# Kernel optimization log

Hardware: AMD Instinct MI355X
Metric: run time of the kernel (lower is better)

Reference implementation:

```python
import jax, jax.numpy as jnp
import numpy as np

GROUP_SIZE = 128


def setup_inputs() -> dict:
    key = jax.random.key(0)
    k1, k2, k3 = jax.random.split(key, 3)
    B, S, IN, OUT = 4, 8192, 1024, 1024
    x = jax.random.normal(k1, (B, S, IN), dtype=jnp.float32)
    weight = jax.random.normal(k2, (OUT, IN), dtype=jnp.float32) * 0.02
    bias = jax.random.normal(k3, (OUT,), dtype=jnp.float32) * 0.01
    return {"x": x, "weight": weight, "bias": bias}


def reference(x, weight, bias):
    """Quantized int8 path: quantize() + _forward_int8 of OneBitLinear.

    - weights binarized to +/-1 int8 (sign, with 0 -> -1, matching
      sign().clamp(min=0) bit packing then 2*bit-1)
    - per-group weight scales = group absmax, stored fp16 (as in quantize())
    - activations dynamically quantized per-token to int8
    - int32-accumulated GEMM, rescaled by x_scale * mean group scale per row
    """
    out_f, in_f = weight.shape
    ng = in_f // GROUP_SIZE
    w_g = weight.reshape(out_f, ng, GROUP_SIZE)
    # per-group absmax scales, cast fp16 -> fp32 to mimic fp16 storage
    scales = jnp.maximum(jnp.max(jnp.abs(w_g), axis=-1), 1e-8)
    scales = scales.astype(jnp.float16).astype(jnp.float32)  # [O, ng]
    # +/-1 int8 weights (sign>0 -> +1, else -1; zero maps to -1 like the packer)
    w_int8 = jnp.where(weight > 0, 1, -1).astype(jnp.int8)  # [O, I]

    # dynamic per-token activation quantization
    x_f = x.reshape(-1, in_f)  # [BT, I]
    x_scale = jnp.maximum(jnp.max(jnp.abs(x_f), axis=1, keepdims=True), 1e-8) / 127.0
    x_int8 = jnp.clip(jnp.round(x_f / x_scale), -128, 127).astype(jnp.int8)

    # int8 GEMM with int32 accumulation
    out_i32 = jnp.matmul(
        x_int8.astype(jnp.int32), w_int8.T.astype(jnp.int32)
    )  # [BT, O]

    w_scale_per_row = jnp.mean(scales, axis=1)  # [O]
    out_f32 = out_i32.astype(jnp.float32) * x_scale * w_scale_per_row[None, :]
    out_f32 = out_f32 + bias[None, :]
    return out_f32.reshape(*x.shape[:-1], out_f)
```

## Files before the change

kernel.cpp:

```cpp
#include <hip/hip_runtime.h>
#include <hip/hip_fp16.h>

#define K_DIM 1024
#define N_DIM 1024

typedef int v4i __attribute__((ext_vector_type(4)));

__device__ __forceinline__ void async_load16(const void* g, void* l) {
    __builtin_amdgcn_global_load_lds(
        (const __attribute__((address_space(1))) unsigned int*)g,
        (__attribute__((address_space(3))) unsigned int*)l,
        16, 0, 0);
}

__global__ __launch_bounds__(256) void prep_quant(const float* __restrict__ w,
                                                  const float* __restrict__ x,
                                                  signed char* __restrict__ wq,
                                                  float* __restrict__ wscale,
                                                  signed char* __restrict__ xq,
                                                  float* __restrict__ xs) {
    const int lane = threadIdx.x & 63;
    if (blockIdx.x < 256) {
        const int row = blockIdx.x * 4 + (threadIdx.x >> 6);
        const float4* wr = (const float4*)(w + (size_t)row * K_DIM);
        float4 v[4];
#pragma unroll
        for (int j = 0; j < 4; ++j) v[j] = wr[lane * 4 + j];

        float g = 0.f;
#pragma unroll
        for (int j = 0; j < 4; ++j) {
            g = fmaxf(g, fabsf(v[j].x)); g = fmaxf(g, fabsf(v[j].y));
            g = fmaxf(g, fabsf(v[j].z)); g = fmaxf(g, fabsf(v[j].w));
        }
        g = fmaxf(g, __shfl_xor(g, 1, 64));
        g = fmaxf(g, __shfl_xor(g, 2, 64));
        g = fmaxf(g, __shfl_xor(g, 4, 64));
        const float s = __half2float(__float2half(fmaxf(g, 1e-8f)));
        float t = s;
        t += __shfl_xor(t, 8, 64);
        t += __shfl_xor(t, 16, 64);
        t += __shfl_xor(t, 32, 64);
        if (lane == 0) wscale[row] = t * 0.125f;

        int pk[4];
#pragma unroll
        for (int j = 0; j < 4; ++j) {
            const int b0 = (v[j].x > 0.f) ? 1 : -1;
            const int b1 = (v[j].y > 0.f) ? 1 : -1;
            const int b2 = (v[j].z > 0.f) ? 1 : -1;
            const int b3 = (v[j].w > 0.f) ? 1 : -1;
            pk[j] = (b0 & 255) | ((b1 & 255) << 8) | ((b2 & 255) << 16) | (b3 << 24);
        }
        *(int4*)(wq + (size_t)row * K_DIM + lane * 16) = make_int4(pk[0], pk[1], pk[2], pk[3]);
    } else {
        const int row = (blockIdx.x - 256) * 4 + (threadIdx.x >> 6);
        const float4* xr = (const float4*)(x + (size_t)row * K_DIM);
        float4 v[4];
#pragma unroll
        for (int j = 0; j < 4; ++j) v[j] = xr[lane * 4 + j];

        float am = 0.f;
#pragma unroll
        for (int j = 0; j < 4; ++j) {
            am = fmaxf(am, fabsf(v[j].x)); am = fmaxf(am, fabsf(v[j].y));
            am = fmaxf(am, fabsf(v[j].z)); am = fmaxf(am, fabsf(v[j].w));
        }
#pragma unroll
        for (int off = 32; off >= 1; off >>= 1) am = fmaxf(am, __shfl_xor(am, off, 64));
        const float scale = fmaxf(am, 1e-8f) / 127.f;
        const float inv   = 1.0f / scale;

        int pk[4];
#pragma unroll
        for (int j = 0; j < 4; ++j) {
            const int b0 = (int)fminf(fmaxf(rintf(v[j].x * inv), -128.f), 127.f);
            const int b1 = (int)fminf(fmaxf(rintf(v[j].y * inv), -128.f), 127.f);
            const int b2 = (int)fminf(fmaxf(rintf(v[j].z * inv), -128.f), 127.f);
            const int b3 = (int)fminf(fmaxf(rintf(v[j].w * inv), -128.f), 127.f);
            pk[j] = (b0 & 255) | ((b1 & 255) << 8) | ((b2 & 255) << 16) | (b3 << 24);
        }
        *(int4*)(xq + (size_t)row * K_DIM + lane * 16) = make_int4(pk[0], pk[1], pk[2], pk[3]);
        if (lane == 0) xs[row] = scale;
    }
}

__global__ __launch_bounds__(512, 2) void gemm_i8(const signed char* __restrict__ A,
                                                  const signed char* __restrict__ Bw,
                                                  const float* __restrict__ xs,
                                                  const float* __restrict__ wscale,
                                                  const float* __restrict__ bias,
                                                  float* __restrict__ out) {
    extern __shared__ __align__(16) signed char Bl[];

    const int tid  = threadIdx.x;
    const int lane = tid & 63;
    const int wave = tid >> 6;
    const int wm   = wave >> 1;
    const int wn   = wave & 1;

    const int bid = blockIdx.x;
    const int xcd = bid & 7;
    const int u   = bid >> 3;
    const int mT  = xcd * 16 + (u >> 3);
    const int nT  = u & 7;
    const size_t mBase = (size_t)mT * 256;
    const int    nBase = nT * 128;

    const int brow   = tid >> 6;
    const int bchunk = (tid & 63) ^ brow;
    const signed char* Bg = Bw + (size_t)(nBase + brow) * K_DIM + bchunk * 16;
#pragma unroll
    for (int c = 0; c < 16; ++c)
        async_load16(Bg + (size_t)(c * 8) * K_DIM, Bl + c * 8192 + tid * 16);

    const int r16 = lane & 15;
    const int g   = lane >> 4;

    const signed char* Arow[4];
#pragma unroll
    for (int mf = 0; mf < 4; ++mf)
        Arow[mf] = A + (mBase + wm * 64 + mf * 16 + r16) * (size_t)K_DIM + g * 16;

    const int s7 = r16 & 7;
    int Bbase[4];
#pragma unroll
    for (int nf = 0; nf < 4; ++nf)
        Bbase[nf] = (wn * 64 + nf * 16 + r16) * 1024;

    __syncthreads();

    v4i acc[4][4] = {};

#pragma unroll
    for (int t = 0; t < 16; ++t) {
        v4i af[4], bf[4];
#pragma unroll
        for (int mf = 0; mf < 4; ++mf)
            af[mf] = *(const v4i*)(Arow[mf] + t * 64);
#pragma unroll
        for (int nf = 0; nf < 4; ++nf)
            bf[nf] = *(const v4i*)(Bl + Bbase[nf] + (((t * 4 + g) ^ s7) * 16));
#pragma unroll
        for (int mf = 0; mf < 4; ++mf)
#pragma unroll
            for (int nf = 0; nf < 4; ++nf)
                acc[mf][nf] = __builtin_amdgcn_mfma_i32_16x16x64_i8(
                    af[mf], bf[nf], acc[mf][nf], 0, 0, 0);
    }

    const int rq = g * 4;
    float xsr[4][4];
#pragma unroll
    for (int mf = 0; mf < 4; ++mf)
#pragma unroll
        for (int i = 0; i < 4; ++i)
            xsr[mf][i] = xs[mBase + wm * 64 + mf * 16 + rq + i];

#pragma unroll
    for (int nf = 0; nf < 4; ++nf) {
        const int col   = nBase + wn * 64 + nf * 16 + r16;
        const float wsc = wscale[col];
        const float bb  = bias[col];
#pragma unroll
        for (int mf = 0; mf < 4; ++mf) {
#pragma unroll
            for (int i = 0; i < 4; ++i) {
                const size_t row = mBase + wm * 64 + mf * 16 + rq + i;
                out[row * N_DIM + col] = (float)acc[mf][nf][i] * xsr[mf][i] * wsc + bb;
            }
        }
    }
}

extern "C" void kernel_launch(void* const* d_in, const int* in_sizes, int n_in,
                              void* d_out, int out_size, void* d_ws, size_t ws_size,
                              hipStream_t stream) {
    const float* x    = (const float*)d_in[0];
    const float* w    = (const float*)d_in[1];
    const float* bias = (const float*)d_in[2];
    float* out = (float*)d_out;

    const int BT = in_sizes[0] / K_DIM;

    char* ws = (char*)d_ws;
    signed char* xq     = (signed char*)ws;
    float*       xs     = (float*)(ws + (size_t)BT * K_DIM);
    signed char* wq     = (signed char*)(ws + (size_t)BT * K_DIM + (size_t)BT * 4);
    float*       wscale = (float*)((char*)wq + (size_t)N_DIM * K_DIM);

    static bool s_attr_set = false;
    if (!s_attr_set) {
        hipFuncSetAttribute((const void*)gemm_i8,
                            hipFuncAttributeMaxDynamicSharedMemorySize, 131072);
        s_attr_set = true;
    }

    prep_quant<<<256 + BT / 4, 256, 0, stream>>>(w, x, wq, wscale, xq, xs);
    gemm_i8<<<(BT / 256) * (N_DIM / 128), 512, 131072, stream>>>(xq, wq, xs, wscale, bias, out);
}
```

Measured before the change: 304.9 us.

## Restructure int8 GEMM into 256x256 tiles with triple-buffered LDS pipeline

The GEMM tile grows from 256x128 to 256x256 per block with 8 waves in a 2x4 layout. A is now staged through LDS instead of read directly from global memory, and the full-K B preload is replaced by a 3-stage ring of 64-wide K slices filled by async global-to-LDS loads. Loads are interleaved with MFMA phases using explicit barriers, waitcnt and setprio. The goal is to overlap memory with compute and improve reuse. In exchange it adds many barriers per iteration and higher register pressure from 32 accumulators per thread.

```diff
diff --git a/kernel.cpp b/kernel.cpp
--- a/kernel.cpp
+++ b/kernel.cpp
@@ -12,6 +12,12 @@
         (__attribute__((address_space(3))) unsigned int*)l,
         16, 0, 0);
 }
+
+#define BAR() do { asm volatile("" ::: "memory"); \
+                   __builtin_amdgcn_s_barrier();  \
+                   asm volatile("" ::: "memory"); } while (0)
+#define LGKM0() do { asm volatile("s_waitcnt lgkmcnt(0)" ::: "memory"); \
+                     __builtin_amdgcn_sched_barrier(0); } while (0)
 
 __global__ __launch_bounds__(256) void prep_quant(const float* __restrict__ w,
                                                   const float* __restrict__ x,
@@ -91,71 +97,127 @@
                                                   const float* __restrict__ wscale,
                                                   const float* __restrict__ bias,
                                                   float* __restrict__ out) {
-    extern __shared__ __align__(16) signed char Bl[];
+    extern __shared__ __align__(16) signed char lds[];
 
     const int tid  = threadIdx.x;
     const int lane = tid & 63;
     const int wave = tid >> 6;
-    const int wm   = wave >> 1;
-    const int wn   = wave & 1;
+    const int wm   = wave >> 2;
+    const int wn   = wave & 3;
 
     const int bid = blockIdx.x;
     const int xcd = bid & 7;
     const int u   = bid >> 3;
-    const int mT  = xcd * 16 + (u >> 3);
-    const int nT  = u & 7;
+    const int mT  = xcd * 16 + (u >> 2);
+    const int nT  = u & 3;
     const size_t mBase = (size_t)mT * 256;
-    const int    nBase = nT * 128;
-
-    const int brow   = tid >> 6;
-    const int bchunk = (tid & 63) ^ brow;
-    const signed char* Bg = Bw + (size_t)(nBase + brow) * K_DIM + bchunk * 16;
-#pragma unroll
-    for (int c = 0; c < 16; ++c)
-        async_load16(Bg + (size_t)(c * 8) * K_DIM, Bl + c * 8192 + tid * 16);
-
-    const int r16 = lane & 15;
-    const int g   = lane >> 4;
-
-    const signed char* Arow[4];
-#pragma unroll
-    for (int mf = 0; mf < 4; ++mf)
-        Arow[mf] = A + (mBase + wm * 64 + mf * 16 + r16) * (size_t)K_DIM + g * 16;
-
-    const int s7 = r16 & 7;
-    int Bbase[4];
+    const int    nBase = nT * 256;
+
+    const int srow = tid >> 2;
+    const int lc16 = ((tid & 3) ^ ((srow >> 1) & 3)) * 16;
+    const int dst  = tid * 16;
+    const signed char* Ag0 = A  + (mBase + srow) * K_DIM + lc16;
+    const signed char* Ag1 = Ag0 + (size_t)128 * K_DIM;
+    const signed char* Bg0 = Bw + (size_t)(nBase + srow) * K_DIM + lc16;
+    const signed char* Bg1 = Bg0 + (size_t)128 * K_DIM;
+
+#define SA0(b, kt) async_load16(Ag0 + (kt) * 64, lds + (b) * 32768 + dst)
+#define SA1(b, kt) async_load16(Ag1 + (kt) * 64, lds + (b) * 32768 + 8192 + dst)
+#define SB0(b, kt) async_load16(Bg0 + (kt) * 64, lds + (b) * 32768 + 16384 + dst)
+#define SB1(b, kt) async_load16(Bg1 + (kt) * 64, lds + (b) * 32768 + 24576 + dst)
+
+    const int r16  = lane & 15;
+    const int g    = lane >> 4;
+    const int phys = (g ^ ((r16 >> 1) & 3)) * 16;
+    int aoff[8], boff[4];
+#pragma unroll
+    for (int mf = 0; mf < 8; ++mf)
+        aoff[mf] = (wm * 128 + mf * 16 + r16) * 64 + phys;
 #pragma unroll
     for (int nf = 0; nf < 4; ++nf)
-        Bbase[nf] = (wn * 64 + nf * 16 + r16) * 1024;
-
-    __syncthreads();
-
-    v4i acc[4][4] = {};
-
-#pragma unroll
+        boff[nf] = 16384 + (wn * 64 + nf * 16 + r16) * 64 + phys;
+
+    v4i acc[8][4] = {};
+
+    SA0(0, 0); SA1(0, 0); SB0(0, 0); SB1(0, 0);
+    SA0(1, 1); SA1(1, 1); SB0(1, 1); SB1(1, 1);
+    asm volatile("s_waitcnt vmcnt(4)" ::: "memory");
+    BAR();
+
     for (int t = 0; t < 16; ++t) {
-        v4i af[4], bf[4];
-#pragma unroll
-        for (int mf = 0; mf < 4; ++mf)
-            af[mf] = *(const v4i*)(Arow[mf] + t * 64);
-#pragma unroll
-        for (int nf = 0; nf < 4; ++nf)
-            bf[nf] = *(const v4i*)(Bl + Bbase[nf] + (((t * 4 + g) ^ s7) * 16));
-#pragma unroll
-        for (int mf = 0; mf < 4; ++mf)
-#pragma unroll
-            for (int nf = 0; nf < 4; ++nf)
-                acc[mf][nf] = __builtin_amdgcn_mfma_i32_16x16x64_i8(
-                    af[mf], bf[nf], acc[mf][nf], 0, 0, 0);
-    }
+        const signed char* Lb = lds + (t % 3) * 32768;
+        const int bn = (t + 2) % 3;
+        const bool st = (t < 14);
+        v4i bf[4], af0, af1;
+
+#pragma unroll
+        for (int nf = 0; nf < 4; ++nf) bf[nf] = *(const v4i*)(Lb + boff[nf]);
+        af0 = *(const v4i*)(Lb + aoff[0]);
+        af1 = *(const v4i*)(Lb + aoff[1]);
+        if (st) SA0(bn, t + 2);
+        BAR(); LGKM0();
+        __builtin_amdgcn_s_setprio(1);
+#pragma unroll
+        for (int nf = 0; nf < 4; ++nf) {
+            acc[0][nf] = __builtin_amdgcn_mfma_i32_16x16x64_i8(af0, bf[nf], acc[0][nf], 0, 0, 0);
+            acc[1][nf] = __builtin_amdgcn_mfma_i32_16x16x64_i8(af1, bf[nf], acc[1][nf], 0, 0, 0);
+        }
+        __builtin_amdgcn_s_setprio(0);
+        BAR();
+
+        af0 = *(const v4i*)(Lb + aoff[2]);
+        af1 = *(const v4i*)(Lb + aoff[3]);
+        if (st) SA1(bn, t + 2);
+        BAR(); LGKM0();
+        __builtin_amdgcn_s_setprio(1);
+#pragma unroll
+        for (int nf = 0; nf < 4; ++nf) {
+            acc[2][nf] = __builtin_amdgcn_mfma_i32_16x16x64_i8(af0, bf[nf], acc[2][nf], 0, 0, 0);
+            acc[3][nf] = __builtin_amdgcn_mfma_i32_16x16x64_i8(af1, bf[nf], acc[3][nf], 0, 0, 0);
+        }
+        __builtin_amdgcn_s_setprio(0);
+        BAR();
+
+        af0 = *(const v4i*)(Lb + aoff[4]);
+        af1 = *(const v4i*)(Lb + aoff[5]);
+        if (st) SB0(bn, t + 2);
+        BAR(); LGKM0();
+        __builtin_amdgcn_s_setprio(1);
+#pragma unroll
+        for (int nf = 0; nf < 4; ++nf) {
+            acc[4][nf] = __builtin_amdgcn_mfma_i32_16x16x64_i8(af0, bf[nf], acc[4][nf], 0, 0, 0);
+            acc[5][nf] = __builtin_amdgcn_mfma_i32_16x16x64_i8(af1, bf[nf], acc[5][nf], 0, 0, 0);
+        }
+        __builtin_amdgcn_s_setprio(0);
+        BAR();
+
+        af0 = *(const v4i*)(Lb + aoff[6]);
+        af1 = *(const v4i*)(Lb + aoff[7]);
+        if (st) SB1(bn, t + 2);
+        BAR(); LGKM0();
+        __builtin_amdgcn_s_setprio(1);
+#pragma unroll
+        for (int nf = 0; nf < 4; ++nf) {
+            acc[6][nf] = __builtin_amdgcn_mfma_i32_16x16x64_i8(af0, bf[nf], acc[6][nf], 0, 0, 0);
+            acc[7][nf] = __builtin_amdgcn_mfma_i32_16x16x64_i8(af1, bf[nf], acc[7][nf], 0, 0, 0);
+        }
+        __builtin_amdgcn_s_setprio(0);
+        if (t < 14) asm volatile("s_waitcnt vmcnt(4)" ::: "memory");
+        else        asm volatile("s_waitcnt vmcnt(0)" ::: "memory");
+        BAR();
+    }
+#undef SA0
+#undef SA1
+#undef SB0
+#undef SB1
 
     const int rq = g * 4;
-    float xsr[4][4];
-#pragma unroll
-    for (int mf = 0; mf < 4; ++mf)
+    float xsr[8][4];
+#pragma unroll
+    for (int mf = 0; mf < 8; ++mf)
 #pragma unroll
         for (int i = 0; i < 4; ++i)
-            xsr[mf][i] = xs[mBase + wm * 64 + mf * 16 + rq + i];
+            xsr[mf][i] = xs[mBase + wm * 128 + mf * 16 + rq + i];
 
 #pragma unroll
     for (int nf = 0; nf < 4; ++nf) {
@@ -163,10 +225,10 @@
         const float wsc = wscale[col];
         const float bb  = bias[col];
 #pragma unroll
-        for (int mf = 0; mf < 4; ++mf) {
+        for (int mf = 0; mf < 8; ++mf) {
 #pragma unroll
             for (int i = 0; i < 4; ++i) {
-                const size_t row = mBase + wm * 64 + mf * 16 + rq + i;
+                const size_t row = mBase + wm * 128 + mf * 16 + rq + i;
                 out[row * N_DIM + col] = (float)acc[mf][nf][i] * xsr[mf][i] * wsc + bb;
             }
         }
@@ -192,10 +254,10 @@
     static bool s_attr_set = false;
     if (!s_attr_set) {
         hipFuncSetAttribute((const void*)gemm_i8,
-                            hipFuncAttributeMaxDynamicSharedMemorySize, 131072);
+                            hipFuncAttributeMaxDynamicSharedMemorySize, 98304);
         s_attr_set = true;
     }
 
     prep_quant<<<256 + BT / 4, 256, 0, stream>>>(w, x, wq, wscale, xq, xs);
-    gemm_i8<<<(BT / 256) * (N_DIM / 128), 512, 131072, stream>>>(xq, wq, xs, wscale, bias, out);
-}
+    gemm_i8<<<(BT / 256) * (N_DIM / 256), 512, 98304, stream>>>(xq, wq, xs, wscale, bias, out);
+}
```

New measurement: 292.3 us. 4.2% less time.

## Stage A and B tiles through double-buffered LDS with 256x256 block tiles

Applied to the files above, without the earlier changes.

The GEMM previously loaded the whole 128-column B slab into LDS once and read A directly from global memory. It now uses 256x256 output tiles and streams both A and B K-slices of 128 bytes through two LDS buffers with asynchronous global-to-LDS loads. The next stage's load overlaps with the MFMAs on the current stage. This aims to improve reuse of A and hide global latency, at the cost of more accumulator registers per wave (8x4 fragments) and a barrier per K step.

```diff
diff --git a/kernel.cpp b/kernel.cpp
--- a/kernel.cpp
+++ b/kernel.cpp
@@ -12,6 +12,10 @@
         (__attribute__((address_space(3))) unsigned int*)l,
         16, 0, 0);
 }
+
+#define BAR() do { asm volatile("" ::: "memory"); \
+                   __builtin_amdgcn_s_barrier();  \
+                   asm volatile("" ::: "memory"); } while (0)
 
 __global__ __launch_bounds__(256) void prep_quant(const float* __restrict__ w,
                                                   const float* __restrict__ x,
@@ -91,71 +95,93 @@
                                                   const float* __restrict__ wscale,
                                                   const float* __restrict__ bias,
                                                   float* __restrict__ out) {
-    extern __shared__ __align__(16) signed char Bl[];
+    extern __shared__ __align__(16) signed char lds[];
 
     const int tid  = threadIdx.x;
     const int lane = tid & 63;
     const int wave = tid >> 6;
-    const int wm   = wave >> 1;
-    const int wn   = wave & 1;
+    const int wm   = wave >> 2;
+    const int wn   = wave & 3;
 
     const int bid = blockIdx.x;
     const int xcd = bid & 7;
     const int u   = bid >> 3;
-    const int mT  = xcd * 16 + (u >> 3);
-    const int nT  = u & 7;
+    const int mT  = xcd * 16 + (u >> 2);
+    const int nT  = u & 3;
     const size_t mBase = (size_t)mT * 256;
-    const int    nBase = nT * 128;
-
-    const int brow   = tid >> 6;
-    const int bchunk = (tid & 63) ^ brow;
-    const signed char* Bg = Bw + (size_t)(nBase + brow) * K_DIM + bchunk * 16;
-#pragma unroll
-    for (int c = 0; c < 16; ++c)
-        async_load16(Bg + (size_t)(c * 8) * K_DIM, Bl + c * 8192 + tid * 16);
+    const int    nBase = nT * 256;
+
+    const int srow = tid >> 3;
+    const int scol = ((tid & 7) ^ (srow & 7)) * 16;
+    const int dst  = tid * 16;
+    const signed char* Ag = A  + (mBase + srow) * K_DIM + scol;
+    const signed char* Bg = Bw + (size_t)(nBase + srow) * K_DIM + scol;
+
+#define STAGE(b, kt) do {                                                     \
+        const int _ko = (kt) * 128;                                           \
+        const int _bb = (b) * 65536;                                          \
+        async_load16(Ag + _ko,                       lds + _bb +         dst);\
+        async_load16(Ag + (size_t) 64 * K_DIM + _ko, lds + _bb +  8192 + dst);\
+        async_load16(Ag + (size_t)128 * K_DIM + _ko, lds + _bb + 16384 + dst);\
+        async_load16(Ag + (size_t)192 * K_DIM + _ko, lds + _bb + 24576 + dst);\
+        async_load16(Bg + _ko,                       lds + _bb + 32768 + dst);\
+        async_load16(Bg + (size_t) 64 * K_DIM + _ko, lds + _bb + 40960 + dst);\
+        async_load16(Bg + (size_t)128 * K_DIM + _ko, lds + _bb + 49152 + dst);\
+        async_load16(Bg + (size_t)192 * K_DIM + _ko, lds + _bb + 57344 + dst);\
+    } while (0)
 
     const int r16 = lane & 15;
     const int g   = lane >> 4;
-
-    const signed char* Arow[4];
-#pragma unroll
-    for (int mf = 0; mf < 4; ++mf)
-        Arow[mf] = A + (mBase + wm * 64 + mf * 16 + r16) * (size_t)K_DIM + g * 16;
-
-    const int s7 = r16 & 7;
-    int Bbase[4];
+    const int c0  = ((g ^ (r16 & 7)) * 16);
+    int aoff[8], boff[4];
+#pragma unroll
+    for (int mf = 0; mf < 8; ++mf)
+        aoff[mf] = (wm * 128 + mf * 16 + r16) * 128 + c0;
 #pragma unroll
     for (int nf = 0; nf < 4; ++nf)
-        Bbase[nf] = (wn * 64 + nf * 16 + r16) * 1024;
-
-    __syncthreads();
-
-    v4i acc[4][4] = {};
-
-#pragma unroll
-    for (int t = 0; t < 16; ++t) {
-        v4i af[4], bf[4];
-#pragma unroll
-        for (int mf = 0; mf < 4; ++mf)
-            af[mf] = *(const v4i*)(Arow[mf] + t * 64);
-#pragma unroll
-        for (int nf = 0; nf < 4; ++nf)
-            bf[nf] = *(const v4i*)(Bl + Bbase[nf] + (((t * 4 + g) ^ s7) * 16));
-#pragma unroll
-        for (int mf = 0; mf < 4; ++mf)
+        boff[nf] = 32768 + (wn * 64 + nf * 16 + r16) * 128 + c0;
+
+    v4i acc[8][4] = {};
+
+    STAGE(0, 0);
+
+    for (int t = 0; t < 8; ++t) {
+        asm volatile("s_waitcnt vmcnt(0)" ::: "memory");
+        BAR();
+        if (t < 7) STAGE((t + 1) & 1, t + 1);
+
+        const signed char* Lb = lds + (t & 1) * 65536;
+
+#pragma unroll
+        for (int ks = 0; ks < 2; ++ks) {
+            const int sx = ks * 64;
+            v4i af[8], bf[4];
+#pragma unroll
+            for (int mf = 0; mf < 8; ++mf)
+                af[mf] = *(const v4i*)(Lb + (aoff[mf] ^ sx));
 #pragma unroll
             for (int nf = 0; nf < 4; ++nf)
-                acc[mf][nf] = __builtin_amdgcn_mfma_i32_16x16x64_i8(
-                    af[mf], bf[nf], acc[mf][nf], 0, 0, 0);
-    }
+                bf[nf] = *(const v4i*)(Lb + (boff[nf] ^ sx));
+#pragma unroll
+            for (int mf = 0; mf < 8; ++mf)
+#pragma unroll
+                for (int nf = 0; nf < 4; ++nf)
+                    acc[mf][nf] = __builtin_amdgcn_mfma_i32_16x16x64_i8(
+                        af[mf], bf[nf], acc[mf][nf], 0, 0, 0);
+        }
+
+        __builtin_amdgcn_sched_barrier(0);
+        asm volatile("s_waitcnt lgkmcnt(0)" ::: "memory");
+    }
+#undef STAGE
 
     const int rq = g * 4;
-    float xsr[4][4];
-#pragma unroll
-    for (int mf = 0; mf < 4; ++mf)
+    float xsr[8][4];
+#pragma unroll
+    for (int mf = 0; mf < 8; ++mf)
 #pragma unroll
         for (int i = 0; i < 4; ++i)
-            xsr[mf][i] = xs[mBase + wm * 64 + mf * 16 + rq + i];
+            xsr[mf][i] = xs[mBase + wm * 128 + mf * 16 + rq + i];
 
 #pragma unroll
     for (int nf = 0; nf < 4; ++nf) {
@@ -163,10 +189,10 @@
         const float wsc = wscale[col];
         const float bb  = bias[col];
 #pragma unroll
-        for (int mf = 0; mf < 4; ++mf) {
+        for (int mf = 0; mf < 8; ++mf) {
 #pragma unroll
             for (int i = 0; i < 4; ++i) {
-                const size_t row = mBase + wm * 64 + mf * 16 + rq + i;
+                const size_t row = mBase + wm * 128 + mf * 16 + rq + i;
                 out[row * N_DIM + col] = (float)acc[mf][nf][i] * xsr[mf][i] * wsc + bb;
             }
         }
@@ -197,5 +223,5 @@
     }
 
     prep_quant<<<256 + BT / 4, 256, 0, stream>>>(w, x, wq, wscale, xq, xs);
-    gemm_i8<<<(BT / 256) * (N_DIM / 128), 512, 131072, stream>>>(xq, wq, xs, wscale, bias, out);
-}
+    gemm_i8<<<(BT / 256) * (N_DIM / 256), 512, 131072, stream>>>(xq, wq, xs, wscale, bias, out);
+}
```

Result: faster. 290.3 us (-4.8%).
